# Kernel tuning notes

Hardware: AMD Instinct MI355X
Metric: run time of the kernel (lower is better)

The kernel has to match this reference:

```python
import jax, jax.numpy as jnp
import numpy as np

N_NODES = 50000
IN_FEATS = 256
OUT_DIM = 64
N_EDGES = 800000


def setup_inputs() -> dict:
    key = jax.random.key(0)
    k1, k2, k3, k4 = jax.random.split(key, 4)
    x = jax.random.normal(k1, (N_NODES, IN_FEATS), dtype=jnp.float32)
    edge_index = jax.random.randint(k2, (2, N_EDGES), 0, N_NODES, dtype=jnp.int64)
    # Glorot-style init for the GCN weight, zeros bias (as in PyG GCNConv)
    scale = jnp.sqrt(6.0 / (IN_FEATS + OUT_DIM)).astype(jnp.float32)
    W = jax.random.uniform(k3, (IN_FEATS, OUT_DIM), dtype=jnp.float32, minval=-1.0, maxval=1.0) * scale
    b = jnp.zeros((OUT_DIM,), dtype=jnp.float32)
    return {"x": x, "edge_index": edge_index, "W": W, "b": b}


def _gcn_relu(x, edge_index, W, b):
    n = x.shape[0]
    # linear transform first (PyG GCNConv): h = x @ W
    h = x @ W  # [N, out_dim]
    # add self-loops
    loops = jnp.arange(n, dtype=edge_index.dtype)
    src = jnp.concatenate([edge_index[0], loops])  # [E+N]
    dst = jnp.concatenate([edge_index[1], loops])
    # symmetric degree normalization: deg over target index with unit weights
    deg = jax.ops.segment_sum(jnp.ones_like(dst, dtype=h.dtype), dst, num_segments=n)
    deg_inv_sqrt = jnp.where(deg > 0, jax.lax.rsqrt(jnp.maximum(deg, 1e-12)), 0.0)
    norm = deg_inv_sqrt[src] * deg_inv_sqrt[dst]  # [E+N]
    # gather source features, scale, scatter-add at destination
    msg = h[src] * norm[:, None]  # [E+N, out_dim]
    agg = jax.ops.segment_sum(msg, dst, num_segments=n)  # [N, out_dim]
    return jax.nn.relu(agg + b)


def reference(x, edge_index, W, b):
    return _gcn_relu(x, edge_index, W, b)
```

## Files before the change

### kernel.cpp

```cpp
#include <hip/hip_runtime.h>
#include <hip/hip_fp16.h>

#define INF    256
#define OUTF   64
#define TSH    7
#define TNODE  128
#define NBMAX  512
#define CAP    3584
#define MS_T   1024
#define MS_EPT 4

typedef __attribute__((ext_vector_type(8))) short bf16x8;
typedef __attribute__((ext_vector_type(4))) float f32x4;

__device__ __forceinline__ short f2bf(float f) {
    union { float f; unsigned int u; } v; v.f = f;
    unsigned int u = v.u;
    u += 0x7FFFu + ((u >> 16) & 1u);
    return (short)(u >> 16);
}

__global__ void init_gcur_kernel(int* __restrict__ gcur, int nbuck) {
    int i = blockIdx.x * blockDim.x + threadIdx.x;
    if (i < nbuck) gcur[i] = i * CAP;
}

__global__ __launch_bounds__(MS_T) void msplit_kernel(
    const int* __restrict__ src, const int* __restrict__ dst,
    int* __restrict__ gcur, int* __restrict__ ebuk, int e, int nbuck)
{
    __shared__ int h[NBMAX], lb[NBMAX];
    const int t = threadIdx.x;
    for (int i = t; i < nbuck; i += MS_T) h[i] = 0;
    __syncthreads();

    const int base = blockIdx.x * (MS_T * MS_EPT);
    const int i0 = base + t * MS_EPT;
    int sv[MS_EPT], dl[MS_EPT], off[MS_EPT], bk[MS_EPT];

    if (i0 + MS_EPT <= e) {
        int4 s0 = *reinterpret_cast<const int4*>(src + i0);
        int4 d0 = *reinterpret_cast<const int4*>(dst + i0);
        sv[0]=s0.x; sv[1]=s0.y; sv[2]=s0.z; sv[3]=s0.w;
        int dd[MS_EPT] = {d0.x,d0.y,d0.z,d0.w};
        #pragma unroll
        for (int k = 0; k < MS_EPT; ++k) {
            bk[k] = dd[k] >> TSH; dl[k] = dd[k] & (TNODE - 1);
            off[k] = atomicAdd(&h[bk[k]], 1);
        }
    } else {
        #pragma unroll
        for (int k = 0; k < MS_EPT; ++k) {
            int i = i0 + k;
            if (i < e) {
                int dd = dst[i];
                sv[k] = src[i]; bk[k] = dd >> TSH; dl[k] = dd & (TNODE - 1);
                off[k] = atomicAdd(&h[bk[k]], 1);
            } else bk[k] = -1;
        }
    }
    __syncthreads();
    for (int i = t; i < nbuck; i += MS_T) lb[i] = h[i] ? atomicAdd(&gcur[i], h[i]) : 0;
    __syncthreads();
    #pragma unroll
    for (int k = 0; k < MS_EPT; ++k) {
        if (bk[k] >= 0) {
            int pos = lb[bk[k]] + off[k];
            if (pos < (bk[k] + 1) * CAP)
                ebuk[pos] = (sv[k] & 0xFFFF) | (dl[k] << 16);
        }
    }
}

__global__ __launch_bounds__(512) void place_kernel(
    const int* __restrict__ gcur, const int* __restrict__ ebuk,
    unsigned short* __restrict__ ecol, int* __restrict__ rowptr,
    unsigned short* __restrict__ pcnt, float* __restrict__ dinv, int n)
{
    __shared__ int h[TNODE];
    __shared__ int lcur[TNODE];
    __shared__ unsigned short outb[CAP];

    const int b = blockIdx.x;
    const int t = threadIdx.x;
    const int nb0 = b << TSH;
    const int nn  = min(TNODE, n - nb0);
    const int beg = b * CAP;
    const int m   = min(gcur[b] - beg, CAP);

    if (t < TNODE) h[t] = 0;
    __syncthreads();
    for (int i = t; i < m; i += 512)
        atomicAdd(&h[(ebuk[beg + i] >> 16) & (TNODE - 1)], 1);
    __syncthreads();

    int v = (t < TNODE) ? h[t] : 0;
    if (t < TNODE) lcur[t] = v;
    __syncthreads();
    #pragma unroll
    for (int o = 1; o < TNODE; o <<= 1) {
        int add = (t < TNODE && t >= o) ? lcur[t - o] : 0;
        __syncthreads();
        if (t < TNODE) lcur[t] += add;
        __syncthreads();
    }
    if (t < TNODE) {
        int excl = lcur[t] - v;
        if (t < nn) {
            rowptr[nb0 + t] = beg + excl;
            pcnt[nb0 + t]   = (unsigned short)v;
            dinv[nb0 + t]   = rsqrtf((float)(v + 1));
        }
        lcur[t] = excl;
    }
    __syncthreads();

    for (int i = t; i < m; i += 512) {
        int p = ebuk[beg + i];
        int o = atomicAdd(&lcur[(p >> 16) & (TNODE - 1)], 1);
        outb[o] = (unsigned short)(p & 0xFFFF);
    }
    __syncthreads();
    for (int i = t; i < m; i += 512) ecol[beg + i] = outb[i];
}

__global__ __launch_bounds__(256, 2) void gemm_mfma_kernel(
    const float* __restrict__ x, const float* __restrict__ W,
    const float* __restrict__ dinv, __half* __restrict__ hp16,
    int n, int ntiles, int wstride)
{
    __shared__ char smem[65536];
    const int lane = threadIdx.x & 63;
    const int wv   = threadIdx.x >> 6;
    const int wid  = blockIdx.x * 4 + wv;
    const int lg   = lane >> 4;
    const int lr   = lane & 15;
    char* buf0 = smem + wv * 16384;
    char* buf1 = buf0 + 8192;

    bf16x8 breg[4][8];
    #pragma unroll
    for (int ct = 0; ct < 4; ++ct) {
        #pragma unroll
        for (int ks = 0; ks < 8; ++ks) {
            const float* wp = W + (size_t)(ks * 32 + lg * 8) * OUTF + ct * 16 + lr;
            bf16x8 f;
            #pragma unroll
            for (int j = 0; j < 8; ++j)
                f[j] = f2bf(wp[(size_t)j * OUTF]);
            breg[ct][ks] = f;
        }
    }

    auto stage_half = [&](const float* xrow0, char* buf) {
        #pragma unroll
        for (int i = 0; i < 8; ++i) {
            int row  = i * 2 + (lane >> 5);
            int colb = (((lane & 31) << 4) ^ ((row & 7) << 4));
            const float* srcp = xrow0 + (size_t)row * INF + (colb >> 2);
            __builtin_amdgcn_global_load_lds(
                (const __attribute__((address_space(1))) void*)srcp,
                (__attribute__((address_space(3))) void*)(buf + i * 1024),
                16, 0, 0);
        }
        asm volatile("" ::: "memory");
    };

    auto compute_half = [&](const char* buf, int khbase,
                            f32x4& acc0, f32x4& acc1, f32x4& acc2, f32x4& acc3) {
        const int m = (lr & 7) << 4;
        #pragma unroll
        for (int ksl = 0; ksl < 4; ++ksl) {
            int logical = lr * 512 + ksl * 128 + lg * 32;
            float4 a0 = *reinterpret_cast<const float4*>(buf + (logical ^ m));
            float4 a1 = *reinterpret_cast<const float4*>(buf + ((logical + 16) ^ m));
            bf16x8 af;
            af[0] = f2bf(a0.x); af[1] = f2bf(a0.y); af[2] = f2bf(a0.z); af[3] = f2bf(a0.w);
            af[4] = f2bf(a1.x); af[5] = f2bf(a1.y); af[6] = f2bf(a1.z); af[7] = f2bf(a1.w);
            acc0 = __builtin_amdgcn_mfma_f32_16x16x32_bf16(af, breg[0][khbase + ksl], acc0, 0, 0, 0);
            acc1 = __builtin_amdgcn_mfma_f32_16x16x32_bf16(af, breg[1][khbase + ksl], acc1, 0, 0, 0);
            acc2 = __builtin_amdgcn_mfma_f32_16x16x32_bf16(af, breg[2][khbase + ksl], acc2, 0, 0, 0);
            acc3 = __builtin_amdgcn_mfma_f32_16x16x32_bf16(af, breg[3][khbase + ksl], acc3, 0, 0, 0);
        }
    };

    for (int t = wid; t < ntiles; t += wstride) {
        const float* xt = x + (size_t)t * 16 * INF;
        stage_half(xt, buf0);
        stage_half(xt + 128, buf1);

        f32x4 acc0 = {0,0,0,0}, acc1 = {0,0,0,0}, acc2 = {0,0,0,0}, acc3 = {0,0,0,0};

        asm volatile("s_waitcnt vmcnt(8)" ::: "memory");
        compute_half(buf0, 0, acc0, acc1, acc2, acc3);

        asm volatile("s_waitcnt vmcnt(0)" ::: "memory");
        compute_half(buf1, 4, acc0, acc1, acc2, acc3);

        #pragma unroll
        for (int reg = 0; reg < 4; ++reg) {
            int row = t * 16 + lg * 4 + reg;
            float di = dinv[row];
            __half* op = hp16 + (size_t)row * OUTF + lr;
            op[0]  = __float2half(acc0[reg] * di);
            op[16] = __float2half(acc1[reg] * di);
            op[32] = __float2half(acc2[reg] * di);
            op[48] = __float2half(acc3[reg] * di);
        }
    }
}

__global__ __launch_bounds__(256) void aggregate_kernel(
    const int* __restrict__ rowptr, const unsigned short* __restrict__ pcnt,
    const unsigned short* __restrict__ ecol, const __half2* __restrict__ hp2,
    const float* __restrict__ dinv, const float* __restrict__ b,
    float* __restrict__ out, int n)
{
    int widx = (int)((blockIdx.x * (size_t)blockDim.x + threadIdx.x) >> 6);
    int lane = threadIdx.x & 63;
    int half = lane >> 5;
    int l    = lane & 31;
    if (widx >= n) return;

    float2 acc = make_float2(0.f, 0.f);
    if (half == 0) {
        float2 v = __half22float2(hp2[(size_t)widx * 32 + l]);
        acc.x = v.x; acc.y = v.y;
    }

    int beg = rowptr[widx];
    int end = beg + pcnt[widx];

    int j = beg + half;
    for (; j + 14 < end; j += 16) {
        int s0 = ecol[j];      int s1 = ecol[j + 2];
        int s2 = ecol[j + 4];  int s3 = ecol[j + 6];
        int s4 = ecol[j + 8];  int s5 = ecol[j + 10];
        int s6 = ecol[j + 12]; int s7 = ecol[j + 14];
        float2 v0 = __half22float2(hp2[(size_t)s0 * 32 + l]);
        float2 v1 = __half22float2(hp2[(size_t)s1 * 32 + l]);
        float2 v2 = __half22float2(hp2[(size_t)s2 * 32 + l]);
        float2 v3 = __half22float2(hp2[(size_t)s3 * 32 + l]);
        float2 v4 = __half22float2(hp2[(size_t)s4 * 32 + l]);
        float2 v5 = __half22float2(hp2[(size_t)s5 * 32 + l]);
        float2 v6 = __half22float2(hp2[(size_t)s6 * 32 + l]);
        float2 v7 = __half22float2(hp2[(size_t)s7 * 32 + l]);
        acc.x += v0.x + v1.x + v2.x + v3.x + v4.x + v5.x + v6.x + v7.x;
        acc.y += v0.y + v1.y + v2.y + v3.y + v4.y + v5.y + v6.y + v7.y;
    }
    for (; j < end; j += 2) {
        float2 v = __half22float2(hp2[(size_t)ecol[j] * 32 + l]);
        acc.x += v.x; acc.y += v.y;
    }

    float hx = __shfl(acc.x, lane | 32, 64);
    float hy = __shfl(acc.y, lane | 32, 64);
    if (half == 0) {
        float di = dinv[widx];
        float2 bb = reinterpret_cast<const float2*>(b)[l];
        float ox = fmaxf((acc.x + hx) * di + bb.x, 0.f);
        float oy = fmaxf((acc.y + hy) * di + bb.y, 0.f);
        reinterpret_cast<float2*>(out)[(size_t)widx * 32 + l] = make_float2(ox, oy);
    }
}

extern "C" void kernel_launch(void* const* d_in, const int* in_sizes, int n_in,
                              void* d_out, int out_size, void* d_ws, size_t ws_size,
                              hipStream_t stream) {
    const float* x    = (const float*)d_in[0];
    const int*   edge = (const int*)d_in[1];
    const float* W    = (const float*)d_in[2];
    const float* b    = (const float*)d_in[3];
    float* out = (float*)d_out;

    const int n = in_sizes[0] / INF;
    const int e = in_sizes[1] / 2;
    const int* src = edge;
    const int* dst = edge + e;
    const int nbuck = (n + TNODE - 1) >> TSH;

    char* wsc = (char*)d_ws;
    size_t off = 0;
    auto alloc = [&](size_t bytes) { char* p = wsc + off; off += (bytes + 511) & ~511ull; return p; };
    int*            gcur   = (int*)   alloc((size_t)NBMAX * 4);
    int*            rowptr = (int*)   alloc((size_t)n * 4);
    unsigned short* pcnt   = (unsigned short*)alloc((size_t)n * 2);
    float*          dinv   = (float*) alloc((size_t)n * 4);
    int*            ebuk   = (int*)   alloc((size_t)nbuck * CAP * 4);
    unsigned short* ecol   = (unsigned short*)alloc((size_t)nbuck * CAP * 2);
    __half*         hp16   = (__half*)alloc((size_t)n * OUTF * 2);

    init_gcur_kernel<<<2, 256, 0, stream>>>(gcur, nbuck);

    {
        int blocks = (e + MS_T * MS_EPT - 1) / (MS_T * MS_EPT);
        msplit_kernel<<<blocks, MS_T, 0, stream>>>(src, dst, gcur, ebuk, e, nbuck);
    }

    place_kernel<<<nbuck, 512, 0, stream>>>(gcur, ebuk, ecol, rowptr, pcnt, dinv, n);

    {
        const int ntiles = (n + 15) / 16;
        const int blocks = 512;
        gemm_mfma_kernel<<<blocks, 256, 0, stream>>>(x, W, dinv, hp16, n, ntiles, blocks * 4);
    }

    aggregate_kernel<<<(n + 3) / 4, 256, 0, stream>>>(rowptr, pcnt, ecol,
        reinterpret_cast<const __half2*>(hp16), dinv, b, out, n);
}
```

Measured before the change: 74.62 us.

## Vectorize bucket placement, add nontemporal loads/stores, shrink split block size

Halves the split kernel's block size. It switches edge, column-index and output accesses to nontemporal loads and stores. The placement kernel now reads bucketed edges as int4 vectors and copies the sorted columns out with 8-byte stores. An extra 4-way unrolled tail loop is added to the aggregation gather. These changes aim to cut per-element memory instruction overhead and cache pollution, at the risk of losing L2 reuse on data read again later.

```diff
diff --git a/kernel.cpp b/kernel.cpp
--- a/kernel.cpp
+++ b/kernel.cpp
@@ -7,11 +7,13 @@
 #define TNODE  128
 #define NBMAX  512
 #define CAP    3584
-#define MS_T   1024
+#define MS_T   512
 #define MS_EPT 4
 
 typedef __attribute__((ext_vector_type(8))) short bf16x8;
 typedef __attribute__((ext_vector_type(4))) float f32x4;
+typedef __attribute__((ext_vector_type(2))) float f32x2;
+typedef __attribute__((ext_vector_type(4))) int   i32x4;
 
 __device__ __forceinline__ short f2bf(float f) {
     union { float f; unsigned int u; } v; v.f = f;
@@ -39,13 +41,12 @@
     int sv[MS_EPT], dl[MS_EPT], off[MS_EPT], bk[MS_EPT];
 
     if (i0 + MS_EPT <= e) {
-        int4 s0 = *reinterpret_cast<const int4*>(src + i0);
-        int4 d0 = *reinterpret_cast<const int4*>(dst + i0);
-        sv[0]=s0.x; sv[1]=s0.y; sv[2]=s0.z; sv[3]=s0.w;
-        int dd[MS_EPT] = {d0.x,d0.y,d0.z,d0.w};
+        i32x4 s0 = __builtin_nontemporal_load(reinterpret_cast<const i32x4*>(src + i0));
+        i32x4 d0 = __builtin_nontemporal_load(reinterpret_cast<const i32x4*>(dst + i0));
         #pragma unroll
         for (int k = 0; k < MS_EPT; ++k) {
-            bk[k] = dd[k] >> TSH; dl[k] = dd[k] & (TNODE - 1);
+            sv[k] = s0[k];
+            bk[k] = d0[k] >> TSH; dl[k] = d0[k] & (TNODE - 1);
             off[k] = atomicAdd(&h[bk[k]], 1);
         }
     } else {
@@ -79,7 +80,7 @@
 {
     __shared__ int h[TNODE];
     __shared__ int lcur[TNODE];
-    __shared__ unsigned short outb[CAP];
+    __shared__ __align__(16) unsigned short outb[CAP];
 
     const int b = blockIdx.x;
     const int t = threadIdx.x;
@@ -90,8 +91,19 @@
 
     if (t < TNODE) h[t] = 0;
     __syncthreads();
-    for (int i = t; i < m; i += 512)
-        atomicAdd(&h[(ebuk[beg + i] >> 16) & (TNODE - 1)], 1);
+    {
+        int i = t * 4;
+        for (; i + 3 < m; i += 2048) {
+            i32x4 q = *reinterpret_cast<const i32x4*>(ebuk + beg + i);
+            atomicAdd(&h[(q[0] >> 16) & (TNODE - 1)], 1);
+            atomicAdd(&h[(q[1] >> 16) & (TNODE - 1)], 1);
+            atomicAdd(&h[(q[2] >> 16) & (TNODE - 1)], 1);
+            atomicAdd(&h[(q[3] >> 16) & (TNODE - 1)], 1);
+        }
+        if (i < m)
+            for (int kk = i; kk < min(i + 4, m); ++kk)
+                atomicAdd(&h[(ebuk[beg + kk] >> 16) & (TNODE - 1)], 1);
+    }
     __syncthreads();
 
     int v = (t < TNODE) ? h[t] : 0;
@@ -115,13 +127,31 @@
     }
     __syncthreads();
 
-    for (int i = t; i < m; i += 512) {
-        int p = ebuk[beg + i];
-        int o = atomicAdd(&lcur[(p >> 16) & (TNODE - 1)], 1);
-        outb[o] = (unsigned short)(p & 0xFFFF);
-    }
-    __syncthreads();
-    for (int i = t; i < m; i += 512) ecol[beg + i] = outb[i];
+    {
+        int i = t * 4;
+        for (; i + 3 < m; i += 2048) {
+            i32x4 q = *reinterpret_cast<const i32x4*>(ebuk + beg + i);
+            #pragma unroll
+            for (int kk = 0; kk < 4; ++kk) {
+                int o = atomicAdd(&lcur[(q[kk] >> 16) & (TNODE - 1)], 1);
+                outb[o] = (unsigned short)(q[kk] & 0xFFFF);
+            }
+        }
+        if (i < m)
+            for (int kk = i; kk < min(i + 4, m); ++kk) {
+                int p = ebuk[beg + kk];
+                int o = atomicAdd(&lcur[(p >> 16) & (TNODE - 1)], 1);
+                outb[o] = (unsigned short)(p & 0xFFFF);
+            }
+    }
+    __syncthreads();
+    {
+        int nv = m >> 2;
+        uint2* dstv = reinterpret_cast<uint2*>(ecol + beg);
+        const uint2* srcv = reinterpret_cast<const uint2*>(outb);
+        for (int i = t; i < nv; i += 512) dstv[i] = srcv[i];
+        for (int i = (nv << 2) + t; i < m; i += 512) ecol[beg + i] = outb[i];
+    }
 }
 
 __global__ __launch_bounds__(256, 2) void gemm_mfma_kernel(
@@ -233,10 +263,14 @@
 
     int j = beg + half;
     for (; j + 14 < end; j += 16) {
-        int s0 = ecol[j];      int s1 = ecol[j + 2];
-        int s2 = ecol[j + 4];  int s3 = ecol[j + 6];
-        int s4 = ecol[j + 8];  int s5 = ecol[j + 10];
-        int s6 = ecol[j + 12]; int s7 = ecol[j + 14];
+        int s0 = __builtin_nontemporal_load(&ecol[j]);
+        int s1 = __builtin_nontemporal_load(&ecol[j + 2]);
+        int s2 = __builtin_nontemporal_load(&ecol[j + 4]);
+        int s3 = __builtin_nontemporal_load(&ecol[j + 6]);
+        int s4 = __builtin_nontemporal_load(&ecol[j + 8]);
+        int s5 = __builtin_nontemporal_load(&ecol[j + 10]);
+        int s6 = __builtin_nontemporal_load(&ecol[j + 12]);
+        int s7 = __builtin_nontemporal_load(&ecol[j + 14]);
         float2 v0 = __half22float2(hp2[(size_t)s0 * 32 + l]);
         float2 v1 = __half22float2(hp2[(size_t)s1 * 32 + l]);
         float2 v2 = __half22float2(hp2[(size_t)s2 * 32 + l]);
@@ -248,8 +282,21 @@
         acc.x += v0.x + v1.x + v2.x + v3.x + v4.x + v5.x + v6.x + v7.x;
         acc.y += v0.y + v1.y + v2.y + v3.y + v4.y + v5.y + v6.y + v7.y;
     }
+    for (; j + 6 < end; j += 8) {
+        int s0 = __builtin_nontemporal_load(&ecol[j]);
+        int s1 = __builtin_nontemporal_load(&ecol[j + 2]);
+        int s2 = __builtin_nontemporal_load(&ecol[j + 4]);
+        int s3 = __builtin_nontemporal_load(&ecol[j + 6]);
+        float2 v0 = __half22float2(hp2[(size_t)s0 * 32 + l]);
+        float2 v1 = __half22float2(hp2[(size_t)s1 * 32 + l]);
+        float2 v2 = __half22float2(hp2[(size_t)s2 * 32 + l]);
+        float2 v3 = __half22float2(hp2[(size_t)s3 * 32 + l]);
+        acc.x += v0.x + v1.x + v2.x + v3.x;
+        acc.y += v0.y + v1.y + v2.y + v3.y;
+    }
     for (; j < end; j += 2) {
-        float2 v = __half22float2(hp2[(size_t)ecol[j] * 32 + l]);
+        int s = __builtin_nontemporal_load(&ecol[j]);
+        float2 v = __half22float2(hp2[(size_t)s * 32 + l]);
         acc.x += v.x; acc.y += v.y;
     }
 
@@ -258,9 +305,11 @@
     if (half == 0) {
         float di = dinv[widx];
         float2 bb = reinterpret_cast<const float2*>(b)[l];
-        float ox = fmaxf((acc.x + hx) * di + bb.x, 0.f);
-        float oy = fmaxf((acc.y + hy) * di + bb.y, 0.f);
-        reinterpret_cast<float2*>(out)[(size_t)widx * 32 + l] = make_float2(ox, oy);
+        f32x2 o;
+        o[0] = fmaxf((acc.x + hx) * di + bb.x, 0.f);
+        o[1] = fmaxf((acc.y + hy) * di + bb.y, 0.f);
+        __builtin_nontemporal_store(o,
+            reinterpret_cast<f32x2*>(out) + (size_t)widx * 32 + l);
     }
 }
 
```

New measurement: 76.81 us. +2.9%, slower.
